# Kernel optimization log

Measured on AMD Instinct MI355X. Metric: run time of the kernel, lower is better.

Reference implementation:

```python
import jax, jax.numpy as jnp
import numpy as np

# Static configuration (mirrors the list of reconstruction_blocks)
B, F, D, H = 16384, 64, 32, 64
CARDS = ([4, 8, 16, 32] * 8) + [1] * 32  # 32 categorical + 32 numerical features
CMAX = max(CARDS)                         # pad all per-feature output dims to CMAX
TOTAL = sum(CARDS)                        # 512 = concat output width
# flat column indices selecting the valid (unpadded) outputs per feature
_flat = np.concatenate([np.arange(c) + f * CMAX for f, c in enumerate(CARDS)])
FLAT_IDX = jnp.asarray(_flat, dtype=jnp.int32)


def setup_inputs() -> dict:
    key = jax.random.key(0)
    k0, k1, k2 = jax.random.split(key, 3)
    return {
        "inputs": jax.random.normal(k0, (B, F, D), dtype=jnp.float32),
        # per-feature hidden layer: Dense(D -> H)
        "W1": jax.random.normal(k1, (F, D, H), dtype=jnp.float32) / np.float32(np.sqrt(D)),
        "b1": jnp.zeros((F, H), dtype=jnp.float32),
        # per-feature output layer, padded to CMAX columns (only CARDS[f] are used)
        "W2": jax.random.normal(k2, (F, H, CMAX), dtype=jnp.float32) / np.float32(np.sqrt(H)),
        "b2": jnp.zeros((F, CMAX), dtype=jnp.float32),
    }


def reference(inputs, W1, b1, W2, b2):
    # Batched grouped-GEMM over all per-feature MLP blocks at once.
    h = jax.nn.relu(jnp.einsum('bfd,fdh->bfh', inputs, W1) + b1)       # [B,F,H]
    out_pad = jnp.einsum('bfh,fhc->bfc', h, W2) + b2                   # [B,F,CMAX]
    # concat of per-feature outputs (varying widths) == gather of valid columns
    return out_pad.reshape(B, F * CMAX)[:, FLAT_IDX]                   # [B,TOTAL]
```

## Files before the change

kernel.cpp:

```cpp
#include <hip/hip_runtime.h>

typedef __attribute__((ext_vector_type(8))) short short8;
typedef __attribute__((ext_vector_type(4))) float f32x4;
typedef __attribute__((ext_vector_type(4))) unsigned short u16x4;

#define DI __device__ __forceinline__

namespace {
constexpr int TOT_ = 512;
constexpr int XROW = 2048;
constexpr int BT_  = 256;
constexpr int NB_  = (16384 / BT_) * 64;
}

DI unsigned short f2bf(float v) {
    __bf16 h = (__bf16)v;
    return __builtin_bit_cast(unsigned short, h);
}

__global__ __launch_bounds__(256, 4)
void recon_kernel(const float* __restrict__ x, const float* __restrict__ W1,
                  const float* __restrict__ b1, const float* __restrict__ W2,
                  const float* __restrict__ b2, float* __restrict__ out)
{
    __shared__ __align__(16) unsigned short w1t[64 * 32];
    __shared__ __align__(16) unsigned short w2t[32 * 64];
    __shared__ __align__(16) unsigned short hb[4][16 * 64];

    const int bid   = blockIdx.x;
    const int f     = (bid >> 3) & 63;
    const int btile = ((bid & 7) << 3) | (bid >> 9);

    const int tid  = threadIdx.x;
    const int lane = tid & 63;
    const int wv   = tid >> 6;
    const int l15  = lane & 15;
    const int kg   = lane >> 4;
    const int swz  = (l15 & 7) << 3;
    const bool catf = (f < 32);

    const int b0 = btile * BT_ + wv * 64;

    f32x4 xa[4][2];
#pragma unroll
    for (int t = 0; t < 4; ++t) {
        const float* xr = x + (size_t)(b0 + t * 16 + l15) * XROW + f * 32 + kg * 8;
        xa[t][0] = *(const f32x4*)xr;
        xa[t][1] = *(const f32x4*)(xr + 4);
    }

    const float* W1f = W1 + f * 2048;
    const float* W2f = W2 + f * 2048;
    {
        const int e0 = tid * 8;
        f32x4 v0 = *(const f32x4*)(W1f + e0);
        f32x4 v1 = *(const f32x4*)(W1f + e0 + 4);
        if (catf) {
            f32x4 u0 = *(const f32x4*)(W2f + e0);
            f32x4 u1 = *(const f32x4*)(W2f + e0 + 4);
#pragma unroll
            for (int j = 0; j < 8; ++j) {
                int e = e0 + j;
                float u = (j < 4) ? u0[j] : u1[j - 4];
                w2t[(e & 31) * 64 + (e >> 5)] = f2bf(u);
            }
        }
#pragma unroll
        for (int j = 0; j < 8; ++j) {
            int e = e0 + j;
            float v = (j < 4) ? v0[j] : v1[j - 4];
            w1t[(e & 63) * 32 + (e >> 6)] = f2bf(v);
        }
    }
    __syncthreads();

    short8 w1b[4];
#pragma unroll
    for (int nt = 0; nt < 4; ++nt)
        w1b[nt] = *(const short8*)&w1t[(nt * 16 + l15) * 32 + kg * 8];

    short8 w2b[2][2] = {};
    if (catf) {
#pragma unroll
        for (int nt = 0; nt < 2; ++nt)
#pragma unroll
            for (int ks = 0; ks < 2; ++ks)
                w2b[nt][ks] = *(const short8*)&w2t[(nt * 16 + l15) * 64 + ks * 32 + kg * 8];
    } else {
#pragma unroll
        for (int ks = 0; ks < 2; ++ks)
#pragma unroll
            for (int j = 0; j < 8; ++j)
                w2b[0][ks][j] = (short)f2bf(W2f[(ks * 32 + kg * 8 + j) * 32]);
    }

    f32x4 b1q[4], b2q[2];
#pragma unroll
    for (int nt = 0; nt < 4; ++nt) b1q[nt] = *(const f32x4*)(b1 + f * 64 + nt * 16 + kg * 4);
#pragma unroll
    for (int nt = 0; nt < 2; ++nt) b2q[nt] = *(const f32x4*)(b2 + f * 32 + nt * 16 + kg * 4);

    int card, off;
    if (catf) { card = 4 << (f & 3); off = (f >> 2) * 60 + card - 4; }
    else      { card = 1;            off = 480 + (f - 32); }

    unsigned short* hw = hb[wv];

#pragma unroll
    for (int t = 0; t < 4; ++t) {
        short8 af;
#pragma unroll
        for (int j = 0; j < 4; ++j) {
            af[j]     = (short)f2bf(xa[t][0][j]);
            af[4 + j] = (short)f2bf(xa[t][1][j]);
        }

        f32x4 c1[4];
#pragma unroll
        for (int nt = 0; nt < 4; ++nt)
            c1[nt] = __builtin_amdgcn_mfma_f32_16x16x32_bf16(w1b[nt], af, b1q[nt], 0, 0, 0);

#pragma unroll
        for (int nt = 0; nt < 4; ++nt) {
            u16x4 hv;
#pragma unroll
            for (int j = 0; j < 4; ++j) {
                float v = c1[nt][j];
                hv[j] = f2bf(v > 0.f ? v : 0.f);
            }
            *(u16x4*)&hw[(l15 * 64 + nt * 16 + kg * 4) ^ swz] = hv;
        }

        short8 ha[2];
#pragma unroll
        for (int ks = 0; ks < 2; ++ks)
            ha[ks] = *(const short8*)&hw[(l15 * 64 + ks * 32 + kg * 8) ^ swz];

        f32x4 c2[2];
        c2[0] = __builtin_amdgcn_mfma_f32_16x16x32_bf16(w2b[0][0], ha[0], b2q[0], 0, 0, 0);
        c2[0] = __builtin_amdgcn_mfma_f32_16x16x32_bf16(w2b[0][1], ha[1], c2[0], 0, 0, 0);
        if (card == 32) {
            c2[1] = __builtin_amdgcn_mfma_f32_16x16x32_bf16(w2b[1][0], ha[0], b2q[1], 0, 0, 0);
            c2[1] = __builtin_amdgcn_mfma_f32_16x16x32_bf16(w2b[1][1], ha[1], c2[1], 0, 0, 0);
        }

        const int row = b0 + t * 16 + l15;
        if (card > 1) {
            const int ntiles = (card == 32) ? 2 : 1;
            for (int nt = 0; nt < ntiles; ++nt) {
                if (kg * 4 < card - nt * 16) {
                    f32x4 v;
#pragma unroll
                    for (int j = 0; j < 4; ++j) v[j] = c2[nt][j];
                    *(f32x4*)(out + (size_t)row * TOT_ + off + nt * 16 + kg * 4) = v;
                }
            }
        } else {
            if (kg == 0)
                out[(size_t)row * TOT_ + off] = c2[0][0];
        }
    }
}

extern "C" void kernel_launch(void* const* d_in, const int* in_sizes, int n_in,
                              void* d_out, int out_size, void* d_ws, size_t ws_size,
                              hipStream_t stream) {
    const float* x  = (const float*)d_in[0];
    const float* W1 = (const float*)d_in[1];
    const float* b1 = (const float*)d_in[2];
    const float* W2 = (const float*)d_in[3];
    const float* b2 = (const float*)d_in[4];
    float* out = (float*)d_out;
    recon_kernel<<<NB_, 256, 0, stream>>>(x, W1, b1, W2, b2, out);
}
```

Before: 40.19 us.

## Double block row tile and software-pipeline x loads two tiles ahead

Each block now covers 512 batch rows instead of 256, so each wave runs 8 row sub-tiles and the per-feature weight staging into shared memory is spread over twice the work. The x tile loads become a two-deep rolling prefetch inside the loop instead of all being loaded up front, and the launch bounds ask for 6 blocks per CU. The grid halves and the XCD-aware block-to-row mapping is updated. The risk is fewer blocks to fill the GPU and more register pressure, which the higher occupancy hint may not cover.

```diff
diff --git a/kernel.cpp b/kernel.cpp
--- a/kernel.cpp
+++ b/kernel.cpp
@@ -9,8 +9,8 @@
 namespace {
 constexpr int TOT_ = 512;
 constexpr int XROW = 2048;
-constexpr int BT_  = 256;
-constexpr int NB_  = (16384 / BT_) * 64;
+constexpr int RPB  = 512;
+constexpr int NB_  = (16384 / RPB) * 64;
 }
 
 DI unsigned short f2bf(float v) {
@@ -18,7 +18,7 @@
     return __builtin_bit_cast(unsigned short, h);
 }
 
-__global__ __launch_bounds__(256, 4)
+__global__ __launch_bounds__(256, 6)
 void recon_kernel(const float* __restrict__ x, const float* __restrict__ W1,
                   const float* __restrict__ b1, const float* __restrict__ W2,
                   const float* __restrict__ b2, float* __restrict__ out)
@@ -27,9 +27,11 @@
     __shared__ __align__(16) unsigned short w2t[32 * 64];
     __shared__ __align__(16) unsigned short hb[4][16 * 64];
 
-    const int bid   = blockIdx.x;
-    const int f     = (bid >> 3) & 63;
-    const int btile = ((bid & 7) << 3) | (bid >> 9);
+    const int bid = blockIdx.x;
+    const int xcd = bid & 7;
+    const int ii  = bid >> 3;
+    const int f   = ii & 63;
+    const int rg  = (xcd << 2) | (ii >> 6);
 
     const int tid  = threadIdx.x;
     const int lane = tid & 63;
@@ -39,14 +41,15 @@
     const int swz  = (l15 & 7) << 3;
     const bool catf = (f < 32);
 
-    const int b0 = btile * BT_ + wv * 64;
+    const int r0 = rg * RPB + wv * 128;
+    const float* xb = x + (size_t)(r0 + l15) * XROW + f * 32 + kg * 8;
 
-    f32x4 xa[4][2];
+    f32x4 xs[2][2];
 #pragma unroll
-    for (int t = 0; t < 4; ++t) {
-        const float* xr = x + (size_t)(b0 + t * 16 + l15) * XROW + f * 32 + kg * 8;
-        xa[t][0] = *(const f32x4*)xr;
-        xa[t][1] = *(const f32x4*)(xr + 4);
+    for (int s = 0; s < 2; ++s) {
+        const float* p = xb + (size_t)(s * 16) * XROW;
+        xs[s][0] = *(const f32x4*)p;
+        xs[s][1] = *(const f32x4*)(p + 4);
     }
 
     const float* W1f = W1 + f * 2048;
@@ -107,12 +110,18 @@
     unsigned short* hw = hb[wv];
 
 #pragma unroll
-    for (int t = 0; t < 4; ++t) {
+    for (int t = 0; t < 8; ++t) {
+        const int s = t & 1;
         short8 af;
 #pragma unroll
         for (int j = 0; j < 4; ++j) {
-            af[j]     = (short)f2bf(xa[t][0][j]);
-            af[4 + j] = (short)f2bf(xa[t][1][j]);
+            af[j]     = (short)f2bf(xs[s][0][j]);
+            af[4 + j] = (short)f2bf(xs[s][1][j]);
+        }
+        if (t + 2 < 8) {
+            const float* p = xb + (size_t)((t + 2) * 16) * XROW;
+            xs[s][0] = *(const f32x4*)p;
+            xs[s][1] = *(const f32x4*)(p + 4);
         }
 
         f32x4 c1[4];
@@ -144,7 +153,7 @@
             c2[1] = __builtin_amdgcn_mfma_f32_16x16x32_bf16(w2b[1][1], ha[1], c2[1], 0, 0, 0);
         }
 
-        const int row = b0 + t * 16 + l15;
+        const int row = r0 + t * 16 + l15;
         if (card > 1) {
             const int ntiles = (card == 32) ? 2 : 1;
             for (int nt = 0; nt < ntiles; ++nt) {
```

Result: slower. 83.82 us (+108.6%).

## Pre-convert weights to bf16 transposed layout in a separate prep kernel

Applied to the files above, without the earlier changes.

Adds a small prep kernel that converts W1 and W2 to bf16 once per call, transposes them, and writes them to workspace. The main kernel then loads MFMA operand fragments straight from global memory, with no per-block fp32 conversion, LDS staging or __syncthreads. The intent is to cut redundant per-block weight conversion and the barrier from 4096 blocks. The cost is an extra kernel launch, and launch_bounds drops the min-blocks hint.

```diff
diff --git a/kernel.cpp b/kernel.cpp
--- a/kernel.cpp
+++ b/kernel.cpp
@@ -18,13 +18,33 @@
     return __builtin_bit_cast(unsigned short, h);
 }
 
-__global__ __launch_bounds__(256, 4)
-void recon_kernel(const float* __restrict__ x, const float* __restrict__ W1,
-                  const float* __restrict__ b1, const float* __restrict__ W2,
-                  const float* __restrict__ b2, float* __restrict__ out)
+__global__ __launch_bounds__(256)
+void prep_kernel(const float* __restrict__ W1, const float* __restrict__ W2,
+                 unsigned short* __restrict__ ws)
 {
-    __shared__ __align__(16) unsigned short w1t[64 * 32];
-    __shared__ __align__(16) unsigned short w2t[32 * 64];
+    __shared__ __align__(16) unsigned short w1t[2048];
+    __shared__ __align__(16) unsigned short w2t[2048];
+    const int f = blockIdx.x, tid = threadIdx.x, e0 = tid * 8;
+    const float* W1f = W1 + f * 2048;
+    const float* W2f = W2 + f * 2048;
+    f32x4 v0 = *(const f32x4*)(W1f + e0), v1 = *(const f32x4*)(W1f + e0 + 4);
+    f32x4 u0 = *(const f32x4*)(W2f + e0), u1 = *(const f32x4*)(W2f + e0 + 4);
+#pragma unroll
+    for (int j = 0; j < 8; ++j) {
+        int e = e0 + j;
+        w1t[(e & 63) * 32 + (e >> 6)] = f2bf(j < 4 ? v0[j] : v1[j - 4]);
+        w2t[(e & 31) * 64 + (e >> 5)] = f2bf(j < 4 ? u0[j] : u1[j - 4]);
+    }
+    __syncthreads();
+    *(short8*)(ws + f * 2048 + e0)          = *(const short8*)(w1t + e0);
+    *(short8*)(ws + 131072 + f * 2048 + e0) = *(const short8*)(w2t + e0);
+}
+
+__global__ __launch_bounds__(256)
+void recon_kernel(const float* __restrict__ x, const unsigned short* __restrict__ ws,
+                  const float* __restrict__ b1, const float* __restrict__ b2,
+                  float* __restrict__ out)
+{
     __shared__ __align__(16) unsigned short hb[4][16 * 64];
 
     const int bid   = blockIdx.x;
@@ -39,8 +59,35 @@
     const int swz  = (l15 & 7) << 3;
     const bool catf = (f < 32);
 
+    const unsigned short* ws1 = ws + f * 2048;
+    const unsigned short* ws2 = ws + 131072 + f * 2048;
+
+    short8 w1b[4];
+#pragma unroll
+    for (int nt = 0; nt < 4; ++nt)
+        w1b[nt] = *(const short8*)&ws1[(nt * 16 + l15) * 32 + kg * 8];
+
+    short8 w2b[2][2];
+    if (catf) {
+#pragma unroll
+        for (int nt = 0; nt < 2; ++nt)
+#pragma unroll
+            for (int ks = 0; ks < 2; ++ks)
+                w2b[nt][ks] = *(const short8*)&ws2[(nt * 16 + l15) * 64 + ks * 32 + kg * 8];
+    } else {
+#pragma unroll
+        for (int ks = 0; ks < 2; ++ks)
+            w2b[0][ks] = *(const short8*)&ws2[ks * 32 + kg * 8];
+        w2b[1][0] = w2b[0][0]; w2b[1][1] = w2b[0][1];
+    }
+
+    f32x4 b1q[4], b2q[2];
+#pragma unroll
+    for (int nt = 0; nt < 4; ++nt) b1q[nt] = *(const f32x4*)(b1 + f * 64 + nt * 16 + kg * 4);
+#pragma unroll
+    for (int nt = 0; nt < 2; ++nt) b2q[nt] = *(const f32x4*)(b2 + f * 32 + nt * 16 + kg * 4);
+
     const int b0 = btile * BT_ + wv * 64;
-
     f32x4 xa[4][2];
 #pragma unroll
     for (int t = 0; t < 4; ++t) {
@@ -48,57 +95,6 @@
         xa[t][0] = *(const f32x4*)xr;
         xa[t][1] = *(const f32x4*)(xr + 4);
     }
-
-    const float* W1f = W1 + f * 2048;
-    const float* W2f = W2 + f * 2048;
-    {
-        const int e0 = tid * 8;
-        f32x4 v0 = *(const f32x4*)(W1f + e0);
-        f32x4 v1 = *(const f32x4*)(W1f + e0 + 4);
-        if (catf) {
-            f32x4 u0 = *(const f32x4*)(W2f + e0);
-            f32x4 u1 = *(const f32x4*)(W2f + e0 + 4);
-#pragma unroll
-            for (int j = 0; j < 8; ++j) {
-                int e = e0 + j;
-                float u = (j < 4) ? u0[j] : u1[j - 4];
-                w2t[(e & 31) * 64 + (e >> 5)] = f2bf(u);
-            }
-        }
-#pragma unroll
-        for (int j = 0; j < 8; ++j) {
-            int e = e0 + j;
-            float v = (j < 4) ? v0[j] : v1[j - 4];
-            w1t[(e & 63) * 32 + (e >> 6)] = f2bf(v);
-        }
-    }
-    __syncthreads();
-
-    short8 w1b[4];
-#pragma unroll
-    for (int nt = 0; nt < 4; ++nt)
-        w1b[nt] = *(const short8*)&w1t[(nt * 16 + l15) * 32 + kg * 8];
-
-    short8 w2b[2][2] = {};
-    if (catf) {
-#pragma unroll
-        for (int nt = 0; nt < 2; ++nt)
-#pragma unroll
-            for (int ks = 0; ks < 2; ++ks)
-                w2b[nt][ks] = *(const short8*)&w2t[(nt * 16 + l15) * 64 + ks * 32 + kg * 8];
-    } else {
-#pragma unroll
-        for (int ks = 0; ks < 2; ++ks)
-#pragma unroll
-            for (int j = 0; j < 8; ++j)
-                w2b[0][ks][j] = (short)f2bf(W2f[(ks * 32 + kg * 8 + j) * 32]);
-    }
-
-    f32x4 b1q[4], b2q[2];
-#pragma unroll
-    for (int nt = 0; nt < 4; ++nt) b1q[nt] = *(const f32x4*)(b1 + f * 64 + nt * 16 + kg * 4);
-#pragma unroll
-    for (int nt = 0; nt < 2; ++nt) b2q[nt] = *(const f32x4*)(b2 + f * 32 + nt * 16 + kg * 4);
 
     int card, off;
     if (catf) { card = 4 << (f & 3); off = (f >> 2) * 60 + card - 4; }
@@ -171,5 +167,7 @@
     const float* W2 = (const float*)d_in[3];
     const float* b2 = (const float*)d_in[4];
     float* out = (float*)d_out;
-    recon_kernel<<<NB_, 256, 0, stream>>>(x, W1, b1, W2, b2, out);
+    unsigned short* ws = (unsigned short*)d_ws;
+    prep_kernel<<<64, 256, 0, stream>>>(W1, W2, ws);
+    recon_kernel<<<NB_, 256, 0, stream>>>(x, ws, b1, b2, out);
 }
```

New measurement: 45.12 us. 12.3% more time.

## Make blocks persistent over four batch tiles with register-prefetched input loads

Applied to the files above, without the earlier changes.

The grid shrinks from 4096 to 1024 blocks. Each block now handles one feature across four batch tiles, so the per-feature weight staging and bf16 conversion is paid once per four tiles. Inside the loop, the input loads for the next tile are issued while the current tile's MFMAs run, which hides global-load latency. The change also stages W2 into shared memory unconditionally and reads the numerical-feature column from LDS instead of strided global loads, and it drops the occupancy hint from launch bounds. The costs are fewer blocks for latency hiding, higher register pressure from the prefetch buffers, and a different tile-to-block mapping that may affect cache locality.

```diff
diff --git a/kernel.cpp b/kernel.cpp
--- a/kernel.cpp
+++ b/kernel.cpp
@@ -9,8 +9,7 @@
 namespace {
 constexpr int TOT_ = 512;
 constexpr int XROW = 2048;
-constexpr int BT_  = 256;
-constexpr int NB_  = (16384 / BT_) * 64;
+constexpr int NB_  = 1024;
 }
 
 DI unsigned short f2bf(float v) {
@@ -18,7 +17,7 @@
     return __builtin_bit_cast(unsigned short, h);
 }
 
-__global__ __launch_bounds__(256, 4)
+__global__ __launch_bounds__(256)
 void recon_kernel(const float* __restrict__ x, const float* __restrict__ W1,
                   const float* __restrict__ b1, const float* __restrict__ W2,
                   const float* __restrict__ b2, float* __restrict__ out)
@@ -27,9 +26,9 @@
     __shared__ __align__(16) unsigned short w2t[32 * 64];
     __shared__ __align__(16) unsigned short hb[4][16 * 64];
 
-    const int bid   = blockIdx.x;
-    const int f     = (bid >> 3) & 63;
-    const int btile = ((bid & 7) << 3) | (bid >> 9);
+    const int bid = blockIdx.x;
+    const int f   = bid & 63;
+    const int bq  = bid >> 6;
 
     const int tid  = threadIdx.x;
     const int lane = tid & 63;
@@ -39,37 +38,34 @@
     const int swz  = (l15 & 7) << 3;
     const bool catf = (f < 32);
 
-    const int b0 = btile * BT_ + wv * 64;
+    const float* xcol = x + f * 32 + kg * 8;
 
-    f32x4 xa[4][2];
+    f32x4 xs[4][2];
+    {
+        const int rb = bq * 256 + wv * 64 + l15;
 #pragma unroll
-    for (int t = 0; t < 4; ++t) {
-        const float* xr = x + (size_t)(b0 + t * 16 + l15) * XROW + f * 32 + kg * 8;
-        xa[t][0] = *(const f32x4*)xr;
-        xa[t][1] = *(const f32x4*)(xr + 4);
+        for (int t = 0; t < 4; ++t) {
+            const float* p = xcol + (size_t)(rb + t * 16) * XROW;
+            xs[t][0] = *(const f32x4*)p;
+            xs[t][1] = *(const f32x4*)(p + 4);
+        }
     }
 
-    const float* W1f = W1 + f * 2048;
-    const float* W2f = W2 + f * 2048;
     {
         const int e0 = tid * 8;
+        const float* W1f = W1 + f * 2048;
+        const float* W2f = W2 + f * 2048;
         f32x4 v0 = *(const f32x4*)(W1f + e0);
         f32x4 v1 = *(const f32x4*)(W1f + e0 + 4);
-        if (catf) {
-            f32x4 u0 = *(const f32x4*)(W2f + e0);
-            f32x4 u1 = *(const f32x4*)(W2f + e0 + 4);
-#pragma unroll
-            for (int j = 0; j < 8; ++j) {
-                int e = e0 + j;
-                float u = (j < 4) ? u0[j] : u1[j - 4];
-                w2t[(e & 31) * 64 + (e >> 5)] = f2bf(u);
-            }
-        }
+        f32x4 u0 = *(const f32x4*)(W2f + e0);
+        f32x4 u1 = *(const f32x4*)(W2f + e0 + 4);
 #pragma unroll
         for (int j = 0; j < 8; ++j) {
             int e = e0 + j;
             float v = (j < 4) ? v0[j] : v1[j - 4];
             w1t[(e & 63) * 32 + (e >> 6)] = f2bf(v);
+            float u = (j < 4) ? u0[j] : u1[j - 4];
+            w2t[(e & 31) * 64 + (e >> 5)] = f2bf(u);
         }
     }
     __syncthreads();
@@ -89,9 +85,7 @@
     } else {
 #pragma unroll
         for (int ks = 0; ks < 2; ++ks)
-#pragma unroll
-            for (int j = 0; j < 8; ++j)
-                w2b[0][ks][j] = (short)f2bf(W2f[(ks * 32 + kg * 8 + j) * 32]);
+            w2b[0][ks] = *(const short8*)&w2t[ks * 32 + kg * 8];
     }
 
     f32x4 b1q[4], b2q[2];
@@ -107,57 +101,67 @@
     unsigned short* hw = hb[wv];
 
 #pragma unroll
-    for (int t = 0; t < 4; ++t) {
-        short8 af;
+    for (int j = 0; j < 4; ++j) {
+        const int r0 = (bq + j * 16) * 256 + wv * 64;
 #pragma unroll
-        for (int j = 0; j < 4; ++j) {
-            af[j]     = (short)f2bf(xa[t][0][j]);
-            af[4 + j] = (short)f2bf(xa[t][1][j]);
-        }
+        for (int t = 0; t < 4; ++t) {
+            short8 af;
+#pragma unroll
+            for (int q = 0; q < 4; ++q) {
+                af[q]     = (short)f2bf(xs[t][0][q]);
+                af[4 + q] = (short)f2bf(xs[t][1][q]);
+            }
+            if (j < 3) {
+                const float* p = xcol + (size_t)((bq + (j + 1) * 16) * 256
+                                                 + wv * 64 + t * 16 + l15) * XROW;
+                xs[t][0] = *(const f32x4*)p;
+                xs[t][1] = *(const f32x4*)(p + 4);
+            }
 
-        f32x4 c1[4];
+            f32x4 c1[4];
 #pragma unroll
-        for (int nt = 0; nt < 4; ++nt)
-            c1[nt] = __builtin_amdgcn_mfma_f32_16x16x32_bf16(w1b[nt], af, b1q[nt], 0, 0, 0);
+            for (int nt = 0; nt < 4; ++nt)
+                c1[nt] = __builtin_amdgcn_mfma_f32_16x16x32_bf16(w1b[nt], af, b1q[nt], 0, 0, 0);
 
 #pragma unroll
-        for (int nt = 0; nt < 4; ++nt) {
-            u16x4 hv;
+            for (int nt = 0; nt < 4; ++nt) {
+                u16x4 hv;
 #pragma unroll
-            for (int j = 0; j < 4; ++j) {
-                float v = c1[nt][j];
-                hv[j] = f2bf(v > 0.f ? v : 0.f);
+                for (int q = 0; q < 4; ++q) {
+                    float v = c1[nt][q];
+                    hv[q] = f2bf(v > 0.f ? v : 0.f);
+                }
+                *(u16x4*)&hw[(l15 * 64 + nt * 16 + kg * 4) ^ swz] = hv;
             }
-            *(u16x4*)&hw[(l15 * 64 + nt * 16 + kg * 4) ^ swz] = hv;
-        }
 
-        short8 ha[2];
+            short8 ha[2];
 #pragma unroll
-        for (int ks = 0; ks < 2; ++ks)
-            ha[ks] = *(const short8*)&hw[(l15 * 64 + ks * 32 + kg * 8) ^ swz];
+            for (int ks = 0; ks < 2; ++ks)
+                ha[ks] = *(const short8*)&hw[(l15 * 64 + ks * 32 + kg * 8) ^ swz];
 
-        f32x4 c2[2];
-        c2[0] = __builtin_amdgcn_mfma_f32_16x16x32_bf16(w2b[0][0], ha[0], b2q[0], 0, 0, 0);
-        c2[0] = __builtin_amdgcn_mfma_f32_16x16x32_bf16(w2b[0][1], ha[1], c2[0], 0, 0, 0);
-        if (card == 32) {
-            c2[1] = __builtin_amdgcn_mfma_f32_16x16x32_bf16(w2b[1][0], ha[0], b2q[1], 0, 0, 0);
-            c2[1] = __builtin_amdgcn_mfma_f32_16x16x32_bf16(w2b[1][1], ha[1], c2[1], 0, 0, 0);
-        }
+            f32x4 c2[2];
+            c2[0] = __builtin_amdgcn_mfma_f32_16x16x32_bf16(w2b[0][0], ha[0], b2q[0], 0, 0, 0);
+            c2[0] = __builtin_amdgcn_mfma_f32_16x16x32_bf16(w2b[0][1], ha[1], c2[0], 0, 0, 0);
+            if (card == 32) {
+                c2[1] = __builtin_amdgcn_mfma_f32_16x16x32_bf16(w2b[1][0], ha[0], b2q[1], 0, 0, 0);
+                c2[1] = __builtin_amdgcn_mfma_f32_16x16x32_bf16(w2b[1][1], ha[1], c2[1], 0, 0, 0);
+            }
 
-        const int row = b0 + t * 16 + l15;
-        if (card > 1) {
-            const int ntiles = (card == 32) ? 2 : 1;
-            for (int nt = 0; nt < ntiles; ++nt) {
-                if (kg * 4 < card - nt * 16) {
-                    f32x4 v;
+            const int row = r0 + t * 16 + l15;
+            if (card > 1) {
+                const int ntiles = (card == 32) ? 2 : 1;
+                for (int nt = 0; nt < ntiles; ++nt) {
+                    if (kg * 4 < card - nt * 16) {
+                        f32x4 v;
 #pragma unroll
-                    for (int j = 0; j < 4; ++j) v[j] = c2[nt][j];
-                    *(f32x4*)(out + (size_t)row * TOT_ + off + nt * 16 + kg * 4) = v;
+                        for (int q = 0; q < 4; ++q) v[q] = c2[nt][q];
+                        *(f32x4*)(out + (size_t)row * TOT_ + off + nt * 16 + kg * 4) = v;
+                    }
                 }
+            } else {
+                if (kg == 0)
+                    out[(size_t)row * TOT_ + off] = c2[0][0];
             }
-        } else {
-            if (kg == 0)
-                out[(size_t)row * TOT_ + off] = c2[0][0];
         }
     }
 }
```

Result: slower. 49.73 us (+23.8%).
